# Optimization experiments

Hardware: AMD Instinct MI355X
Metric: run time of the kernel (lower is better)

The kernel has to match this reference:

```python
import jax, jax.numpy as jnp
import numpy as np

N = 8192      # number of tokens/nodes
D = 256       # out_dim
E = N - 1     # one dependency triple per non-root node
ALPHA = 0.2   # LeakyReLU negative slope


def setup_inputs() -> dict:
    key = jax.random.key(0)
    k1, k2, k3, k4 = jax.random.split(key, 4)
    x = jax.random.normal(k1, (N, D), jnp.float32)
    W = jax.random.normal(k2, (D, D), jnp.float32) / np.sqrt(D)      # nn.Linear(out,out,bias=False).weight
    a = jax.random.normal(k3, (2 * D,), jnp.float32) / np.sqrt(2 * D)  # nn.Linear(2*out,1,bias=False).weight
    # each node 1..N-1 is a dependent exactly once -> h_dict keys are [0,1,...,N-1] in order
    dep = jnp.arange(1, N, dtype=jnp.int32)
    # each governor appears at most once -> each e_tensor row is softmaxed exactly once
    gov = jax.random.permutation(k4, N)[:E].astype(jnp.int32)
    return {"x": x, "W": W, "a": a, "dep": dep, "gov": gov}


def reference(x, W, a, dep, gov):
    Nn, Dd = x.shape
    neg_big = jnp.asarray(-1e18, x.dtype)
    Hx = x @ W.T  # self.weight(x[i]) for every node, [N, D]
    # per-edge attention logit: attn_weight(cat(W x_gov, W x_dep))
    s = jnp.concatenate([Hx[gov], Hx[dep]], axis=-1) @ a  # [E]
    # dense e_tensor exactly as in the module
    e = jnp.zeros((Nn, Nn), x.dtype).at[gov, dep].set(s)
    # rows belonging to a governor get masked softmax; other rows untouched
    gov_mask = jnp.zeros((Nn,), bool).at[gov].set(True)
    masked = jnp.where(e > 0, e, neg_big)
    sm = jax.nn.softmax(masked, axis=1)
    attn = jnp.where(gov_mask[:, None], sm, e)
    # self_loop/h_dict init: h[dep] = W x[gov]; node 0 stays zeros
    h = jnp.zeros((Nn, Dd), x.dtype).at[dep].set(Hx[gov])
    # aggregation: h[gov] += attn[gov, dep] * W x[dep]
    coef = attn[gov, dep]  # [E]
    h = h + jax.ops.segment_sum(coef[:, None] * Hx[dep], gov, num_segments=Nn)
    return jax.nn.leaky_relu(h, ALPHA)
```

## Files before the change

kernel.cpp:

```cpp
#include <hip/hip_runtime.h>

#define D 256
#define BM 64
#define BN 64
#define BK 32
#define LDA (BM + 4)
#define LDB (BN + 4)

__global__ __launch_bounds__(256) void gemm_xwt(
    const float* __restrict__ X, const float* __restrict__ W,
    float* __restrict__ Hx) {
  __shared__ float As[BK][LDA];
  __shared__ float Bs[BK][LDB];
  const int bm = blockIdx.x * BM;
  const int bn = blockIdx.y * BN;
  const int t = threadIdx.x;
  const int tx = t & 15, ty = t >> 4;
  const int lrow = t >> 3, lc4 = t & 7;

  float acc[4][4] = {};

  for (int k0 = 0; k0 < D; k0 += BK) {
#pragma unroll
    for (int rr = 0; rr < BM; rr += 32) {
      int r = lrow + rr;
      float4 v = *(const float4*)&X[(size_t)(bm + r) * D + k0 + lc4 * 4];
      As[lc4 * 4 + 0][r] = v.x; As[lc4 * 4 + 1][r] = v.y;
      As[lc4 * 4 + 2][r] = v.z; As[lc4 * 4 + 3][r] = v.w;
    }
#pragma unroll
    for (int rr = 0; rr < BN; rr += 32) {
      int r = lrow + rr;
      float4 v = *(const float4*)&W[(size_t)(bn + r) * D + k0 + lc4 * 4];
      Bs[lc4 * 4 + 0][r] = v.x; Bs[lc4 * 4 + 1][r] = v.y;
      Bs[lc4 * 4 + 2][r] = v.z; Bs[lc4 * 4 + 3][r] = v.w;
    }
    __syncthreads();
#pragma unroll
    for (int kk = 0; kk < BK; ++kk) {
      float4 a4 = *(const float4*)&As[kk][ty * 4];
      float4 b4 = *(const float4*)&Bs[kk][tx * 4];
      float av[4] = {a4.x, a4.y, a4.z, a4.w};
      float bv[4] = {b4.x, b4.y, b4.z, b4.w};
#pragma unroll
      for (int i = 0; i < 4; ++i)
#pragma unroll
        for (int jj = 0; jj < 4; ++jj)
          acc[i][jj] = fmaf(av[i], bv[jj], acc[i][jj]);
    }
    __syncthreads();
  }

#pragma unroll
  for (int i = 0; i < 4; ++i) {
    float4 o = make_float4(acc[i][0], acc[i][1], acc[i][2], acc[i][3]);
    *(float4*)&Hx[(size_t)(bm + ty * 4 + i) * D + bn + tx * 4] = o;
  }
}

__global__ void scatter_inv(const int* __restrict__ gov, int* __restrict__ inv, int E) {
  int e = blockIdx.x * 256 + threadIdx.x;
  if (e < E) inv[gov[e]] = e;
}

__global__ __launch_bounds__(256) void finalize(
    const float* __restrict__ Hx, const float* __restrict__ a,
    const int* __restrict__ gov, const int* __restrict__ inv,
    float* __restrict__ out) {
  const int j = blockIdx.x;
  const int c = threadIdx.x;

  float h = 0.f;
  if (j > 0) {
    int g = gov[j - 1];
    h = Hx[(size_t)g * D + c];
  }

  const int e2 = inv[j];
  if (e2 >= 0) {
    const int d = e2 + 1;
    const float hd = Hx[(size_t)d * D + c];
    float p = Hx[(size_t)j * D + c] * a[c] + hd * a[D + c];
#pragma unroll
    for (int off = 32; off > 0; off >>= 1) p += __shfl_down(p, off);
    __shared__ float red[4];
    const int lane = threadIdx.x & 63, wv = threadIdx.x >> 6;
    if (lane == 0) red[wv] = p;
    __syncthreads();
    const float s = red[0] + red[1] + red[2] + red[3];
    const float coef = (s > 0.f) ? 1.f : (1.f / 8192.f);
    h += coef * hd;
  }

  out[(size_t)j * D + c] = (h >= 0.f) ? h : 0.2f * h;
}

extern "C" void kernel_launch(void* const* d_in, const int* in_sizes, int n_in,
                              void* d_out, int out_size, void* d_ws, size_t ws_size,
                              hipStream_t stream) {
  const float* x = (const float*)d_in[0];
  const float* W = (const float*)d_in[1];
  const float* a = (const float*)d_in[2];
  const int* gov = (const int*)d_in[4];
  const int E = in_sizes[4];
  const int N = E + 1;

  float* Hx = (float*)d_ws;
  int* inv = (int*)((char*)d_ws + (size_t)N * D * sizeof(float));

  hipMemsetAsync(inv, 0xFF, (size_t)N * sizeof(int), stream);
  hipLaunchKernelGGL(scatter_inv, dim3((E + 255) / 256), dim3(256), 0, stream,
                     gov, inv, E);
  hipLaunchKernelGGL(gemm_xwt, dim3(N / BM, D / BN), dim3(256), 0, stream,
                     x, W, Hx);
  hipLaunchKernelGGL(finalize, dim3(N), dim3(D), 0, stream,
                     Hx, a, gov, inv, (float*)d_out);
}
```

Measured before the change: 98.45 us.

## Use bf16 MFMA GEMM, precompute attention projections, vectorize finalize

Replaces the fp32 FMA GEMM with a bf16 MFMA 16x16x32 GEMM that converts inputs while staging them in LDS. Attention logits are now computed algebraically as x·(W^T a1) and x·(W^T a2), using a single-block prep kernel plus a per-row dot kernel. This removes the block reduction in finalize, which now handles four rows per block with float4 accesses. The memset and scatter launch are folded into prep. Converting to bf16 reduces GEMM precision, and the single-block prep kernel plus the extra pq launch add serial overhead.

```diff
diff --git a/kernel.cpp b/kernel.cpp
--- a/kernel.cpp
+++ b/kernel.cpp
@@ -1,98 +1,164 @@
 #include <hip/hip_runtime.h>
+#include <hip/hip_bf16.h>
 
-#define D 256
-#define BM 64
+#define NN 8192
+#define DD 256
+#define EE (NN - 1)
+
+typedef __attribute__((ext_vector_type(8))) short bf16x8;
+typedef __attribute__((ext_vector_type(4))) float f32x4;
+
+__device__ inline unsigned short f2bf(float f) {
+  return __builtin_bit_cast(unsigned short, __float2bfloat16(f));
+}
+
+__global__ __launch_bounds__(1024) void prep(
+    const float* __restrict__ W, const float* __restrict__ a,
+    const int* __restrict__ gov,
+    float* __restrict__ u, float* __restrict__ v, int* __restrict__ inv) {
+  const int t = threadIdx.x;
+  const int k = t & 255, part = t >> 8;
+
+  for (int i = t; i < NN; i += 1024) inv[i] = -1;
+  __syncthreads();
+  for (int e = t; e < EE; e += 1024) inv[gov[e]] = e;
+
+  float up = 0.f, vp = 0.f;
+  const int j0 = part * 64;
+  for (int j = j0; j < j0 + 64; ++j) {
+    float w = W[(size_t)j * DD + k];
+    up = fmaf(a[j], w, up);
+    vp = fmaf(a[DD + j], w, vp);
+  }
+  __shared__ float redu[4][256], redv[4][256];
+  redu[part][k] = up; redv[part][k] = vp;
+  __syncthreads();
+  if (t < 256) {
+    u[t] = redu[0][t] + redu[1][t] + redu[2][t] + redu[3][t];
+    v[t] = redv[0][t] + redv[1][t] + redv[2][t] + redv[3][t];
+  }
+}
+
+__global__ __launch_bounds__(256) void pq_kernel(
+    const float* __restrict__ x, const float* __restrict__ u,
+    const float* __restrict__ v, float* __restrict__ p, float* __restrict__ q) {
+  const int wid = threadIdx.x >> 6, lane = threadIdx.x & 63;
+  const int row = blockIdx.x * 4 + wid;
+  const float4 xv = *(const float4*)&x[(size_t)row * DD + lane * 4];
+  const float4 uv = *(const float4*)&u[lane * 4];
+  const float4 vv = *(const float4*)&v[lane * 4];
+  float ps = xv.x * uv.x + xv.y * uv.y + xv.z * uv.z + xv.w * uv.w;
+  float qs = xv.x * vv.x + xv.y * vv.y + xv.z * vv.z + xv.w * vv.w;
+#pragma unroll
+  for (int off = 32; off; off >>= 1) {
+    ps += __shfl_xor(ps, off);
+    qs += __shfl_xor(qs, off);
+  }
+  if (lane == 0) { p[row] = ps; q[row] = qs; }
+}
+
+#define BM 128
 #define BN 64
 #define BK 32
-#define LDA (BM + 4)
-#define LDB (BN + 4)
+#define LDAB 40
 
-__global__ __launch_bounds__(256) void gemm_xwt(
+__global__ __launch_bounds__(256) void gemm_mfma(
     const float* __restrict__ X, const float* __restrict__ W,
     float* __restrict__ Hx) {
-  __shared__ float As[BK][LDA];
-  __shared__ float Bs[BK][LDB];
-  const int bm = blockIdx.x * BM;
-  const int bn = blockIdx.y * BN;
+  __shared__ unsigned short As[BM][LDAB];
+  __shared__ unsigned short Bs[BN][LDAB];
   const int t = threadIdx.x;
-  const int tx = t & 15, ty = t >> 4;
-  const int lrow = t >> 3, lc4 = t & 7;
+  const int bm = blockIdx.x * BM, bn = blockIdx.y * BN;
+  const int lane = t & 63;
+  const int wid = t >> 6;
+  const int wr = wid >> 1, wc = wid & 1;
+  const int l15 = lane & 15, l4 = lane >> 4;
 
-  float acc[4][4] = {};
+  f32x4 acc[4][2] = {};
 
-  for (int k0 = 0; k0 < D; k0 += BK) {
+  const int arow = t >> 1, ahalf = t & 1;
+  const int brow = t >> 2, bq = t & 3;
+
+  for (int k0 = 0; k0 < DD; k0 += BK) {
+    {
+      const float* src = &X[(size_t)(bm + arow) * DD + k0 + ahalf * 16];
 #pragma unroll
-    for (int rr = 0; rr < BM; rr += 32) {
-      int r = lrow + rr;
-      float4 v = *(const float4*)&X[(size_t)(bm + r) * D + k0 + lc4 * 4];
-      As[lc4 * 4 + 0][r] = v.x; As[lc4 * 4 + 1][r] = v.y;
-      As[lc4 * 4 + 2][r] = v.z; As[lc4 * 4 + 3][r] = v.w;
+      for (int i = 0; i < 4; ++i) {
+        float4 f = *(const float4*)(src + i * 4);
+        ushort4 pk;
+        pk.x = f2bf(f.x); pk.y = f2bf(f.y); pk.z = f2bf(f.z); pk.w = f2bf(f.w);
+        *(ushort4*)&As[arow][ahalf * 16 + i * 4] = pk;
+      }
     }
+    {
+      const float* src = &W[(size_t)(bn + brow) * DD + k0 + bq * 8];
 #pragma unroll
-    for (int rr = 0; rr < BN; rr += 32) {
-      int r = lrow + rr;
-      float4 v = *(const float4*)&W[(size_t)(bn + r) * D + k0 + lc4 * 4];
-      Bs[lc4 * 4 + 0][r] = v.x; Bs[lc4 * 4 + 1][r] = v.y;
-      Bs[lc4 * 4 + 2][r] = v.z; Bs[lc4 * 4 + 3][r] = v.w;
+      for (int i = 0; i < 2; ++i) {
+        float4 f = *(const float4*)(src + i * 4);
+        ushort4 pk;
+        pk.x = f2bf(f.x); pk.y = f2bf(f.y); pk.z = f2bf(f.z); pk.w = f2bf(f.w);
+        *(ushort4*)&Bs[brow][bq * 8 + i * 4] = pk;
+      }
     }
     __syncthreads();
+
+    bf16x8 af[4], bfr[2];
 #pragma unroll
-    for (int kk = 0; kk < BK; ++kk) {
-      float4 a4 = *(const float4*)&As[kk][ty * 4];
-      float4 b4 = *(const float4*)&Bs[kk][tx * 4];
-      float av[4] = {a4.x, a4.y, a4.z, a4.w};
-      float bv[4] = {b4.x, b4.y, b4.z, b4.w};
+    for (int mf = 0; mf < 4; ++mf)
+      af[mf] = *(const bf16x8*)&As[wr * 64 + mf * 16 + l15][l4 * 8];
 #pragma unroll
-      for (int i = 0; i < 4; ++i)
+    for (int nf = 0; nf < 2; ++nf)
+      bfr[nf] = *(const bf16x8*)&Bs[wc * 32 + nf * 16 + l15][l4 * 8];
 #pragma unroll
-        for (int jj = 0; jj < 4; ++jj)
-          acc[i][jj] = fmaf(av[i], bv[jj], acc[i][jj]);
-    }
+    for (int mf = 0; mf < 4; ++mf)
+#pragma unroll
+      for (int nf = 0; nf < 2; ++nf)
+        acc[mf][nf] = __builtin_amdgcn_mfma_f32_16x16x32_bf16(
+            af[mf], bfr[nf], acc[mf][nf], 0, 0, 0);
     __syncthreads();
   }
 
 #pragma unroll
-  for (int i = 0; i < 4; ++i) {
-    float4 o = make_float4(acc[i][0], acc[i][1], acc[i][2], acc[i][3]);
-    *(float4*)&Hx[(size_t)(bm + ty * 4 + i) * D + bn + tx * 4] = o;
-  }
-}
-
-__global__ void scatter_inv(const int* __restrict__ gov, int* __restrict__ inv, int E) {
-  int e = blockIdx.x * 256 + threadIdx.x;
-  if (e < E) inv[gov[e]] = e;
+  for (int mf = 0; mf < 4; ++mf)
+#pragma unroll
+    for (int nf = 0; nf < 2; ++nf)
+#pragma unroll
+      for (int r = 0; r < 4; ++r) {
+        const int row = bm + wr * 64 + mf * 16 + l4 * 4 + r;
+        const int col = bn + wc * 32 + nf * 16 + l15;
+        Hx[(size_t)row * DD + col] = acc[mf][nf][r];
+      }
 }
 
 __global__ __launch_bounds__(256) void finalize(
-    const float* __restrict__ Hx, const float* __restrict__ a,
-    const int* __restrict__ gov, const int* __restrict__ inv,
-    float* __restrict__ out) {
-  const int j = blockIdx.x;
-  const int c = threadIdx.x;
+    const float* __restrict__ Hx, const float* __restrict__ p,
+    const float* __restrict__ q, const int* __restrict__ gov,
+    const int* __restrict__ inv, float* __restrict__ out) {
+  const int sub = threadIdx.x >> 6, c4 = threadIdx.x & 63;
+  const int j = blockIdx.x * 4 + sub;
 
-  float h = 0.f;
+  float4 h = make_float4(0.f, 0.f, 0.f, 0.f);
   if (j > 0) {
-    int g = gov[j - 1];
-    h = Hx[(size_t)g * D + c];
+    const int g = gov[j - 1];
+    h = *(const float4*)&Hx[(size_t)g * DD + c4 * 4];
   }
-
   const int e2 = inv[j];
   if (e2 >= 0) {
     const int d = e2 + 1;
-    const float hd = Hx[(size_t)d * D + c];
-    float p = Hx[(size_t)j * D + c] * a[c] + hd * a[D + c];
-#pragma unroll
-    for (int off = 32; off > 0; off >>= 1) p += __shfl_down(p, off);
-    __shared__ float red[4];
-    const int lane = threadIdx.x & 63, wv = threadIdx.x >> 6;
-    if (lane == 0) red[wv] = p;
-    __syncthreads();
-    const float s = red[0] + red[1] + red[2] + red[3];
+    const float4 hd = *(const float4*)&Hx[(size_t)d * DD + c4 * 4];
+    const float s = p[j] + q[d];
     const float coef = (s > 0.f) ? 1.f : (1.f / 8192.f);
-    h += coef * hd;
+    h.x = fmaf(coef, hd.x, h.x);
+    h.y = fmaf(coef, hd.y, h.y);
+    h.z = fmaf(coef, hd.z, h.z);
+    h.w = fmaf(coef, hd.w, h.w);
   }
-
-  out[(size_t)j * D + c] = (h >= 0.f) ? h : 0.2f * h;
+  float4 o;
+  o.x = (h.x >= 0.f) ? h.x : 0.2f * h.x;
+  o.y = (h.y >= 0.f) ? h.y : 0.2f * h.y;
+  o.z = (h.z >= 0.f) ? h.z : 0.2f * h.z;
+  o.w = (h.w >= 0.f) ? h.w : 0.2f * h.w;
+  *(float4*)&out[(size_t)j * DD + c4 * 4] = o;
 }
 
 extern "C" void kernel_launch(void* const* d_in, const int* in_sizes, int n_in,
@@ -102,17 +168,18 @@
   const float* W = (const float*)d_in[1];
   const float* a = (const float*)d_in[2];
   const int* gov = (const int*)d_in[4];
-  const int E = in_sizes[4];
-  const int N = E + 1;
 
   float* Hx = (float*)d_ws;
-  int* inv = (int*)((char*)d_ws + (size_t)N * D * sizeof(float));
+  float* p  = Hx + (size_t)NN * DD;
+  float* q  = p + NN;
+  float* u  = q + NN;
+  float* v  = u + DD;
+  int* inv  = (int*)(v + DD);
 
-  hipMemsetAsync(inv, 0xFF, (size_t)N * sizeof(int), stream);
-  hipLaunchKernelGGL(scatter_inv, dim3((E + 255) / 256), dim3(256), 0, stream,
-                     gov, inv, E);
-  hipLaunchKernelGGL(gemm_xwt, dim3(N / BM, D / BN), dim3(256), 0, stream,
+  hipLaunchKernelGGL(prep, dim3(1), dim3(1024), 0, stream, W, a, gov, u, v, inv);
+  hipLaunchKernelGGL(pq_kernel, dim3(NN / 4), dim3(256), 0, stream, x, u, v, p, q);
+  hipLaunchKernelGGL(gemm_mfma, dim3(NN / BM, DD / BN), dim3(256), 0, stream,
                      x, W, Hx);
-  hipLaunchKernelGGL(finalize, dim3(N), dim3(D), 0, stream,
-                     Hx, a, gov, inv, (float*)d_out);
+  hipLaunchKernelGGL(finalize, dim3(NN / 4), dim3(256), 0, stream,
+                     Hx, p, q, gov, inv, (float*)d_out);
 }
```

New measurement: 101.4 us. 1.03x slower.
